# Kernel tuning notes

Hardware: AMD Instinct MI355X
Metric: run time of the kernel (lower is better)

## Reference

```python
import jax, jax.numpy as jnp
import numpy as np

B, T, NF, D = 32, 128, 20, 512
S = 5            # num_sample
L = 96           # seq_len per utterance (static)
EPS = 1e-8


def _cosine(a, b):
    # torch.F.cosine_similarity: dot / max(|a|*|b|, eps)
    num = jnp.sum(a * b, axis=-1)
    den = jnp.maximum(
        jnp.sqrt(jnp.sum(a * a, axis=-1)) * jnp.sqrt(jnp.sum(b * b, axis=-1)), EPS
    )
    return num / den


def setup_inputs() -> dict:
    key = jax.random.key(0)
    output = jax.random.normal(key, (B, T, NF, D), dtype=jnp.float32)

    # static segment gather indices: seq_len = L for every utterance
    batch_idx = jnp.asarray(np.repeat(np.arange(B), L), dtype=jnp.int32)
    time_idx = jnp.asarray(np.tile(np.arange(L), B), dtype=jnp.int32)

    # negative frame indices: for anchor frame i, sample S frames from
    # {0..NF-1} \ {i-1, i, i+1} (matches masked randperm sampling)
    rng = np.random.default_rng(0)
    neg = np.empty((NF - 1, S), dtype=np.int32)
    all_f = np.arange(NF)
    for i in range(NF - 1):
        allowed = all_f[(all_f != i - 1) & (all_f != i) & (all_f != i + 1)]
        neg[i] = rng.permutation(allowed)[:S]
    neg_idx = jnp.asarray(neg.reshape(-1), dtype=jnp.int32)  # [(NF-1)*S]

    return {"output": output, "batch_idx": batch_idx, "time_idx": time_idx,
            "neg_idx": neg_idx}


def reference(output, batch_idx, time_idx, neg_idx):
    # gather valid segments: [num_seg, NF, D]
    seg = output[batch_idx, time_idx]

    anchors = seg[:, :-1, :]                      # [num_seg, NF-1, D]
    sim_pos = _cosine(anchors, seg[:, 1:, :])     # [num_seg, NF-1]

    # negatives[seg, i, s] = seg[seg, neg_idx[i*S+s]]
    negs = seg[:, neg_idx, :].reshape(seg.shape[0], NF - 1, S, D)
    sim_neg = _cosine(anchors[:, :, None, :], negs)          # [num_seg, NF-1, S]

    sim_all = jnp.concatenate([sim_pos[..., None], sim_neg], axis=-1)
    loss = jnp.mean(-jax.nn.log_softmax(sim_all, axis=-1)[..., 0])
    return loss
```

## Files before the change

### kernel.cpp

```cpp
#include <hip/hip_runtime.h>
#include <hip/hip_bf16.h>
#include <math.h>

#define B_  32
#define T_  128
#define NF_ 20
#define D_  512
#define S_  5
#define L_  96
#define EPS_ 1e-8f
#define NSEG (B_ * L_)
#define NPOS (NF_ - 1)
#define NELEM (NF_ * D_)
#define RPAD (D_ + 8)
#define GLD 33

typedef short short8 __attribute__((ext_vector_type(8)));
typedef float f32x4  __attribute__((ext_vector_type(4)));

__device__ __forceinline__ unsigned short f2bf(float f) {
  unsigned int u = __float_as_uint(f);
  u += 0x7fffu + ((u >> 16) & 1u);
  return (unsigned short)(u >> 16);
}

__global__ __launch_bounds__(256) void phoneme_ssl_seg_kernel(
    const float* __restrict__ out,
    const int* __restrict__ batch_idx,
    const int* __restrict__ time_idx,
    const int* __restrict__ neg_idx,
    float* __restrict__ partials) {

  __shared__ __align__(16) unsigned short V[NF_ * RPAD];
  __shared__ float G[32 * GLD];

  const int n = blockIdx.x;
  const int b = batch_idx[n];
  const int t = time_idx[n];
  const float* __restrict__ src = out + (size_t)(b * T_ + t) * NELEM;

  const float4* __restrict__ src4 = (const float4*)src;
#pragma unroll
  for (int it = 0; it < 5; ++it) {
    const int c = threadIdx.x + 256 * it;
    const float4 x = src4[2 * c];
    const float4 y = src4[2 * c + 1];
    short8 v;
    v[0] = (short)f2bf(x.x); v[1] = (short)f2bf(x.y);
    v[2] = (short)f2bf(x.z); v[3] = (short)f2bf(x.w);
    v[4] = (short)f2bf(y.x); v[5] = (short)f2bf(y.y);
    v[6] = (short)f2bf(y.z); v[7] = (short)f2bf(y.w);
    const int row = c >> 6;
    const int col = (c & 63) * 8;
    *(short8*)&V[row * RPAD + col] = v;
  }
  __syncthreads();
  if (threadIdx.x >= 64) return;

  {
    const int lane = threadIdx.x;
    const int r = lane & 15;
    const int q = lane >> 4;
    const int row1 = (16 + r > 19) ? 19 : 16 + r;
    const unsigned short* p0 = &V[r    * RPAD + q * 8];
    const unsigned short* p1 = &V[row1 * RPAD + q * 8];
    f32x4 c00 = {0.f, 0.f, 0.f, 0.f}, c01 = c00, c10 = c00, c11 = c00;
#pragma unroll
    for (int ks = 0; ks < D_ / 32; ++ks) {
      const short8 a0 = *(const short8*)(p0 + 32 * ks);
      const short8 a1 = *(const short8*)(p1 + 32 * ks);
      c00 = __builtin_amdgcn_mfma_f32_16x16x32_bf16(a0, a0, c00, 0, 0, 0);
      c01 = __builtin_amdgcn_mfma_f32_16x16x32_bf16(a0, a1, c01, 0, 0, 0);
      c10 = __builtin_amdgcn_mfma_f32_16x16x32_bf16(a1, a0, c10, 0, 0, 0);
      c11 = __builtin_amdgcn_mfma_f32_16x16x32_bf16(a1, a1, c11, 0, 0, 0);
    }
#pragma unroll
    for (int reg = 0; reg < 4; ++reg) {
      const int rr = q * 4 + reg;
      G[rr        * GLD + r]      = c00[reg];
      G[rr        * GLD + 16 + r] = c01[reg];
      G[(16 + rr) * GLD + r]      = c10[reg];
      G[(16 + rr) * GLD + 16 + r] = c11[reg];
    }
  }

  float local = 0.f;
  if (threadIdx.x < NPOS) {
    const int i = threadIdx.x;
    const float na = sqrtf(G[i * GLD + i]);
    float sims[1 + S_];
    {
      const float nb = sqrtf(G[(i + 1) * GLD + (i + 1)]);
      sims[0] = G[i * GLD + (i + 1)] / fmaxf(na * nb, EPS_);
    }
#pragma unroll
    for (int j = 0; j < S_; ++j) {
      const int f = neg_idx[i * S_ + j];
      const float nb = sqrtf(G[f * GLD + f]);
      sims[1 + j] = G[i * GLD + f] / fmaxf(na * nb, EPS_);
    }
    float m = sims[0];
#pragma unroll
    for (int j = 1; j < 1 + S_; ++j) m = fmaxf(m, sims[j]);
    float se = 0.f;
#pragma unroll
    for (int j = 0; j < 1 + S_; ++j) se += expf(sims[j] - m);
    const float lse = m + logf(se);
    local = -(sims[0] - lse);
  }

#pragma unroll
  for (int off = 32; off >= 1; off >>= 1)
    local += __shfl_xor(local, off, 64);
  if (threadIdx.x == 0)
    partials[n] = local;
}

__global__ __launch_bounds__(256) void phoneme_ssl_reduce_kernel(
    const float* __restrict__ partials, float* __restrict__ loss_out) {
  float acc = 0.f;
  for (int i = threadIdx.x; i < NSEG; i += 256) acc += partials[i];
#pragma unroll
  for (int off = 32; off >= 1; off >>= 1)
    acc += __shfl_xor(acc, off, 64);
  __shared__ float ws[4];
  if ((threadIdx.x & 63) == 0) ws[threadIdx.x >> 6] = acc;
  __syncthreads();
  if (threadIdx.x == 0)
    loss_out[0] = (ws[0] + ws[1] + ws[2] + ws[3]) * (1.0f / (float)(NSEG * NPOS));
}

extern "C" void kernel_launch(void* const* d_in, const int* in_sizes, int n_in,
                              void* d_out, int out_size, void* d_ws, size_t ws_size,
                              hipStream_t stream) {
  const float* out_t    = (const float*)d_in[0];
  const int* batch_idx  = (const int*)d_in[1];
  const int* time_idx   = (const int*)d_in[2];
  const int* neg_idx    = (const int*)d_in[3];
  float* loss_out       = (float*)d_out;
  float* partials       = (float*)d_ws;

  phoneme_ssl_seg_kernel<<<NSEG, 256, 0, stream>>>(
      out_t, batch_idx, time_idx, neg_idx, partials);
  phoneme_ssl_reduce_kernel<<<1, 256, 0, stream>>>(partials, loss_out);
}
```

Before: 223.5 us.

## Split Gram MFMA tiles across four waves and pack bf16 conversion

```diff
diff --git a/kernel.cpp b/kernel.cpp
--- a/kernel.cpp
+++ b/kernel.cpp
@@ -18,10 +18,12 @@
 typedef short short8 __attribute__((ext_vector_type(8)));
 typedef float f32x4  __attribute__((ext_vector_type(4)));
 
-__device__ __forceinline__ unsigned short f2bf(float f) {
-  unsigned int u = __float_as_uint(f);
-  u += 0x7fffu + ((u >> 16) & 1u);
-  return (unsigned short)(u >> 16);
+__device__ __forceinline__ unsigned f2bf2(float lo, float hi) {
+  unsigned ulo = __float_as_uint(lo);
+  ulo += 0x7fffu + ((ulo >> 16) & 1u);
+  unsigned uhi = __float_as_uint(hi);
+  uhi += 0x7fffu + ((uhi >> 16) & 1u);
+  return (uhi & 0xffff0000u) | (ulo >> 16);
 }
 
 __global__ __launch_bounds__(256) void phoneme_ssl_seg_kernel(
@@ -45,44 +47,43 @@
     const int c = threadIdx.x + 256 * it;
     const float4 x = src4[2 * c];
     const float4 y = src4[2 * c + 1];
-    short8 v;
-    v[0] = (short)f2bf(x.x); v[1] = (short)f2bf(x.y);
-    v[2] = (short)f2bf(x.z); v[3] = (short)f2bf(x.w);
-    v[4] = (short)f2bf(y.x); v[5] = (short)f2bf(y.y);
-    v[6] = (short)f2bf(y.z); v[7] = (short)f2bf(y.w);
+    uint4 w;
+    w.x = f2bf2(x.x, x.y);
+    w.y = f2bf2(x.z, x.w);
+    w.z = f2bf2(y.x, y.y);
+    w.w = f2bf2(y.z, y.w);
     const int row = c >> 6;
     const int col = (c & 63) * 8;
-    *(short8*)&V[row * RPAD + col] = v;
+    *(uint4*)&V[row * RPAD + col] = w;
+  }
+  __syncthreads();
+
+  {
+    const int wave = threadIdx.x >> 6;
+    const int lane = threadIdx.x & 63;
+    const int r = lane & 15;
+    const int q = lane >> 4;
+    const int rowA = (wave >= 2) ? ((16 + r > 19) ? 19 : 16 + r) : r;
+    const int rowB = (wave & 1)  ? ((16 + r > 19) ? 19 : 16 + r) : r;
+    const unsigned short* pA = &V[rowA * RPAD + q * 8];
+    const unsigned short* pB = &V[rowB * RPAD + q * 8];
+    f32x4 acc = {0.f, 0.f, 0.f, 0.f};
+#pragma unroll
+    for (int ks = 0; ks < D_ / 32; ++ks) {
+      const short8 a = *(const short8*)(pA + 32 * ks);
+      const short8 bb = (wave == 0 || wave == 3)
+                          ? a
+                          : *(const short8*)(pB + 32 * ks);
+      acc = __builtin_amdgcn_mfma_f32_16x16x32_bf16(a, bb, acc, 0, 0, 0);
+    }
+    const int rbase = (wave >= 2) ? 16 : 0;
+    const int cbase = (wave & 1) ? 16 : 0;
+#pragma unroll
+    for (int reg = 0; reg < 4; ++reg)
+      G[(rbase + q * 4 + reg) * GLD + cbase + r] = acc[reg];
   }
   __syncthreads();
   if (threadIdx.x >= 64) return;
-
-  {
-    const int lane = threadIdx.x;
-    const int r = lane & 15;
-    const int q = lane >> 4;
-    const int row1 = (16 + r > 19) ? 19 : 16 + r;
-    const unsigned short* p0 = &V[r    * RPAD + q * 8];
-    const unsigned short* p1 = &V[row1 * RPAD + q * 8];
-    f32x4 c00 = {0.f, 0.f, 0.f, 0.f}, c01 = c00, c10 = c00, c11 = c00;
-#pragma unroll
-    for (int ks = 0; ks < D_ / 32; ++ks) {
-      const short8 a0 = *(const short8*)(p0 + 32 * ks);
-      const short8 a1 = *(const short8*)(p1 + 32 * ks);
-      c00 = __builtin_amdgcn_mfma_f32_16x16x32_bf16(a0, a0, c00, 0, 0, 0);
-      c01 = __builtin_amdgcn_mfma_f32_16x16x32_bf16(a0, a1, c01, 0, 0, 0);
-      c10 = __builtin_amdgcn_mfma_f32_16x16x32_bf16(a1, a0, c10, 0, 0, 0);
-      c11 = __builtin_amdgcn_mfma_f32_16x16x32_bf16(a1, a1, c11, 0, 0, 0);
-    }
-#pragma unroll
-    for (int reg = 0; reg < 4; ++reg) {
-      const int rr = q * 4 + reg;
-      G[rr        * GLD + r]      = c00[reg];
-      G[rr        * GLD + 16 + r] = c01[reg];
-      G[(16 + rr) * GLD + r]      = c10[reg];
-      G[(16 + rr) * GLD + 16 + r] = c11[reg];
-    }
-  }
 
   float local = 0.f;
   if (threadIdx.x < NPOS) {
@@ -104,8 +105,8 @@
     for (int j = 1; j < 1 + S_; ++j) m = fmaxf(m, sims[j]);
     float se = 0.f;
 #pragma unroll
-    for (int j = 0; j < 1 + S_; ++j) se += expf(sims[j] - m);
-    const float lse = m + logf(se);
+    for (int j = 0; j < 1 + S_; ++j) se += __expf(sims[j] - m);
+    const float lse = m + __logf(se);
     local = -(sims[0] - lse);
   }
 
```

Result: slower. 228.2 us (+2.1%).
